# Performance work log

Measured on AMD Instinct MI355X. Metric: run time of the kernel, lower is better.

## Reference

```python
import jax, jax.numpy as jnp
import numpy as np

H, C = 2, 128  # heads, per-head channels
NEG_SLOPE = 0.2

N_FACT, N_STATUTE, N_CHARGE = 50000, 2000, 200
D_FACT, D_STATUTE, D_CHARGE = 768, 256, 128
E_M, E_I = 500000, 20000
NUM_CHARGES = 10


def setup_inputs() -> dict:
    key = jax.random.key(0)
    ks = iter(jax.random.split(key, 64))
    d = {}
    d['x_fact'] = jax.random.normal(next(ks), (N_FACT, D_FACT), jnp.float32)
    d['x_statute'] = jax.random.normal(next(ks), (N_STATUTE, D_STATUTE), jnp.float32)
    d['x_charge'] = jax.random.normal(next(ks), (N_CHARGE, D_CHARGE), jnp.float32)

    def gat_params(d_src, d_dst):
        s = 1.0 / np.sqrt(max(d_src, 1))
        return (jax.random.normal(next(ks), (d_src, H * C), jnp.float32) * s,
                jax.random.normal(next(ks), (d_dst, H * C), jnp.float32) * (1.0 / np.sqrt(d_dst)),
                jax.random.normal(next(ks), (H, C), jnp.float32) * 0.1,
                jax.random.normal(next(ks), (H, C), jnp.float32) * 0.1,
                jnp.zeros((H * C,), jnp.float32))
    # relation params: m = fact->statute, rm = statute->fact, i = statute->charge, ri = charge->statute
    (d['Wsrc_m'], d['Wdst_m'], d['asrc_m'], d['adst_m'], d['b_m']) = gat_params(D_FACT, D_STATUTE)
    (d['Wsrc_rm'], d['Wdst_rm'], d['asrc_rm'], d['adst_rm'], d['b_rm']) = gat_params(D_STATUTE, D_FACT)
    (d['Wsrc_i'], d['Wdst_i'], d['asrc_i'], d['adst_i'], d['b_i']) = gat_params(D_STATUTE, D_CHARGE)
    (d['Wsrc_ri'], d['Wdst_ri'], d['asrc_ri'], d['adst_ri'], d['b_ri']) = gat_params(D_CHARGE, D_STATUTE)
    d['Wc'] = jax.random.normal(next(ks), (H * C, NUM_CHARGES), jnp.float32) * (1.0 / np.sqrt(H * C))
    d['bc'] = jnp.zeros((NUM_CHARGES,), jnp.float32)

    d['m_src'] = jax.random.randint(next(ks), (E_M,), 0, N_FACT, jnp.int32)
    d['m_dst'] = jax.random.randint(next(ks), (E_M,), 0, N_STATUTE, jnp.int32)
    d['rm_src'] = jax.random.randint(next(ks), (E_M,), 0, N_STATUTE, jnp.int32)
    d['rm_dst'] = jax.random.randint(next(ks), (E_M,), 0, N_FACT, jnp.int32)
    d['i_src'] = jax.random.randint(next(ks), (E_I,), 0, N_STATUTE, jnp.int32)
    d['i_dst'] = jax.random.randint(next(ks), (E_I,), 0, N_CHARGE, jnp.int32)
    d['ri_src'] = jax.random.randint(next(ks), (E_I,), 0, N_CHARGE, jnp.int32)
    d['ri_dst'] = jax.random.randint(next(ks), (E_I,), 0, N_STATUTE, jnp.int32)
    return d


def gat_conv(xs, xd, Wsrc, Wdst, asrc, adst, bias, src, dst, n_dst):
    # bipartite GATConv, heads=2, concat=True, add_self_loops=False
    hs = (xs @ Wsrc).reshape(-1, H, C)          # [Ns,H,C]
    hd = (xd @ Wdst).reshape(-1, H, C)          # [Nd,H,C]
    als = jnp.einsum('nhc,hc->nh', hs, asrc)    # [Ns,H]
    ald = jnp.einsum('nhc,hc->nh', hd, adst)    # [Nd,H]
    e = jax.nn.leaky_relu(als[src] + ald[dst], NEG_SLOPE)  # [E,H]
    mx = jax.ops.segment_max(e, dst, num_segments=n_dst)
    ex = jnp.exp(e - mx[dst])
    denom = jax.ops.segment_sum(ex, dst, num_segments=n_dst)
    alpha = ex / (denom[dst] + 1e-16)           # segment softmax over dst groups
    msg = alpha[:, :, None] * hs[src]           # [E,H,C]
    out = jax.ops.segment_sum(msg, dst, num_segments=n_dst)
    return out.reshape(n_dst, H * C) + bias


def reference(x_fact, x_statute, x_charge,
              Wsrc_m, Wdst_m, asrc_m, adst_m, b_m,
              Wsrc_rm, Wdst_rm, asrc_rm, adst_rm, b_rm,
              Wsrc_i, Wdst_i, asrc_i, adst_i, b_i,
              Wsrc_ri, Wdst_ri, asrc_ri, adst_ri, b_ri,
              Wc, bc,
              m_src, m_dst, rm_src, rm_dst, i_src, i_dst, ri_src, ri_dst):
    out_st_m = gat_conv(x_fact, x_statute, Wsrc_m, Wdst_m, asrc_m, adst_m, b_m, m_src, m_dst, N_STATUTE)
    out_st_ri = gat_conv(x_charge, x_statute, Wsrc_ri, Wdst_ri, asrc_ri, adst_ri, b_ri, ri_src, ri_dst, N_STATUTE)
    statute_emb = 0.5 * (out_st_m + out_st_ri)  # HeteroConv aggr='mean' (unused downstream)
    fact_emb = gat_conv(x_statute, x_fact, Wsrc_rm, Wdst_rm, asrc_rm, adst_rm, b_rm, rm_src, rm_dst, N_FACT)
    charge_emb = gat_conv(x_statute, x_charge, Wsrc_i, Wdst_i, asrc_i, adst_i, b_i, i_src, i_dst, N_CHARGE)
    del statute_emb, charge_emb  # computed by the module but not used by classifier
    return fact_emb @ Wc + bc    # [N_FACT, NUM_CHARGES]
```

## Files before the change

kernel.cpp:

```cpp
#include <hip/hip_runtime.h>
#include <math.h>

#define NFACT 50000
#define NST   2000
#define DFACT 768
#define HC    256
#define EM    500000
#define NK    10
#define NEG   0.2f
#define NCHUNK 196

__device__ __forceinline__ float lrelu(float x) { return x > 0.f ? x : NEG * x; }

__global__ __launch_bounds__(256) void k_prep(const float* __restrict__ xs,
                                              const float* __restrict__ Wsrc,
                                              const float* __restrict__ asrc,
                                              const float* __restrict__ Wc,
                                              const float* __restrict__ Wdst,
                                              const float* __restrict__ adst,
                                              const float* __restrict__ b_rm,
                                              const float* __restrict__ bc,
                                              float* __restrict__ als,
                                              float* __restrict__ hsW,
                                              float* __restrict__ V,
                                              float* __restrict__ cst,
                                              int* __restrict__ counts) {
    int b = blockIdx.x, t = threadIdx.x;
    if (b < NST) {
        __shared__ float xrow[256];
        __shared__ float hrow[256];
        __shared__ float wsum[4];
        xrow[t] = xs[b * 256 + t];
        __syncthreads();
        float acc = 0.f;
        for (int d = 0; d < 256; ++d) acc += xrow[d] * Wsrc[d * 256 + t];
        float p = acc * asrc[t];
        for (int o = 32; o; o >>= 1) p += __shfl_xor(p, o, 64);
        hrow[t] = acc;
        if ((t & 63) == 0) wsum[t >> 6] = p;
        __syncthreads();
        if (t < 20) {
            int h = t / 10, k = t - h * 10;
            float a = 0.f;
            int base = h * 128;
            for (int c = 0; c < 128; ++c) a += hrow[base + c] * Wc[(base + c) * NK + k];
            hsW[b * 20 + t] = a;
        }
        if (t == 0) { als[b * 2 + 0] = wsum[0] + wsum[1]; als[b * 2 + 1] = wsum[2] + wsum[3]; }
    } else if (b < NST + 6) {
        int i = (b - NST) * 256 + t;
        if (i < DFACT * 2) {
            int d = i >> 1, h = i & 1;
            float acc = 0.f;
            for (int c = 0; c < 128; ++c)
                acc += Wdst[d * 256 + h * 128 + c] * adst[h * 128 + c];
            V[d * 2 + h] = acc;
        }
    } else if (b == NST + 6) {
        if (t < NK) {
            float a = bc[t];
            for (int ch = 0; ch < HC; ++ch) a += b_rm[ch] * Wc[ch * NK + t];
            cst[t] = a;
        }
    } else {
        int i = (b - (NST + 7)) * 256 + t;
        if (i <= NFACT) counts[i] = 0;
    }
}

__global__ void k_hist(const int* __restrict__ dst, int* __restrict__ counts) {
    int e = blockIdx.x * 256 + threadIdx.x;
    if (e < EM) atomicAdd(&counts[dst[e]], 1);
}

__global__ __launch_bounds__(256) void k_scanA(const int* __restrict__ counts,
                                               int* __restrict__ bsum) {
    __shared__ int sd[4];
    int t = threadIdx.x, i = blockIdx.x * 256 + t;
    int c = (i <= NFACT) ? counts[i] : 0;
    int v = c;
    for (int o = 32; o; o >>= 1) v += __shfl_xor(v, o, 64);
    if ((t & 63) == 0) sd[t >> 6] = v;
    __syncthreads();
    if (t == 0) bsum[blockIdx.x] = sd[0] + sd[1] + sd[2] + sd[3];
}

__global__ __launch_bounds__(256) void k_scanBC(const int* __restrict__ counts,
                                                const int* __restrict__ bsum,
                                                int* __restrict__ offs,
                                                int* __restrict__ cursor) {
    __shared__ int sb[256];
    __shared__ int sd[256];
    int t = threadIdx.x, b = blockIdx.x;
    sb[t] = (t < NCHUNK) ? bsum[t] : 0;
    __syncthreads();
    for (int o = 1; o < 256; o <<= 1) {
        int v = (t >= o) ? sb[t - o] : 0;
        __syncthreads();
        sb[t] += v;
        __syncthreads();
    }
    int myoff = (b > 0) ? sb[b - 1] : 0;
    int i = b * 256 + t;
    int c = (i <= NFACT) ? counts[i] : 0;
    sd[t] = c;
    __syncthreads();
    for (int o = 1; o < 256; o <<= 1) {
        int v = (t >= o) ? sd[t - o] : 0;
        __syncthreads();
        sd[t] += v;
        __syncthreads();
    }
    if (i <= NFACT) {
        int excl = myoff + sd[t] - c;
        offs[i] = excl;
        cursor[i] = excl;
    }
}

__global__ void k_scat(const int* __restrict__ src, const int* __restrict__ dst,
                       int* __restrict__ cursor, int* __restrict__ perm_s) {
    int e = blockIdx.x * 256 + threadIdx.x;
    if (e >= EM) return;
    int d = dst[e];
    int pos = atomicAdd(&cursor[d], 1);
    perm_s[pos] = src[e];
}

__global__ __launch_bounds__(256) void k_agg(const float* __restrict__ xf,
                                             const float* __restrict__ V,
                                             const float* __restrict__ hsW,
                                             const int* __restrict__ offs,
                                             const int* __restrict__ perm_s,
                                             const float2* __restrict__ als2,
                                             const float* __restrict__ cst,
                                             float* __restrict__ out) {
    int lane = threadIdx.x & 63, wid = threadIdx.x >> 6;
    int n = blockIdx.x * 4 + wid;

    const float* row = xf + (size_t)n * DFACT;
    float a0 = 0.f, a1 = 0.f;
    #pragma unroll
    for (int r = 0; r < 3; ++r) {
        int j0 = r * 256 + lane * 4;
        const float4 u = *(const float4*)(row + j0);
        a0 += u.x * V[(j0 + 0) * 2 + 0] + u.y * V[(j0 + 1) * 2 + 0]
            + u.z * V[(j0 + 2) * 2 + 0] + u.w * V[(j0 + 3) * 2 + 0];
        a1 += u.x * V[(j0 + 0) * 2 + 1] + u.y * V[(j0 + 1) * 2 + 1]
            + u.z * V[(j0 + 2) * 2 + 1] + u.w * V[(j0 + 3) * 2 + 1];
    }
    for (int o = 32; o; o >>= 1) { a0 += __shfl_xor(a0, o, 64); a1 += __shfl_xor(a1, o, 64); }

    bool live = lane < 20;
    bool h0   = lane < 10;
    float al = h0 ? a0 : a1;
    int beg = offs[n], end = offs[n + 1];

    float acc = 0.f, den = 0.f;
    int j = beg;
    for (; j + 4 <= end; j += 4) {
        int sA = perm_s[j + 0], sB = perm_s[j + 1], sC = perm_s[j + 2], sD = perm_s[j + 3];
        float2 aA = als2[sA], aB = als2[sB], aC = als2[sC], aD = als2[sD];
        float hA = live ? hsW[sA * 20 + lane] : 0.f;
        float hB = live ? hsW[sB * 20 + lane] : 0.f;
        float hC = live ? hsW[sC * 20 + lane] : 0.f;
        float hD = live ? hsW[sD * 20 + lane] : 0.f;
        float wA = __expf(lrelu((h0 ? aA.x : aA.y) + al));
        float wB = __expf(lrelu((h0 ? aB.x : aB.y) + al));
        float wC = __expf(lrelu((h0 ? aC.x : aC.y) + al));
        float wD = __expf(lrelu((h0 ? aD.x : aD.y) + al));
        den += (wA + wB) + (wC + wD);
        acc += wA * hA + wB * hB + wC * hC + wD * hD;
    }
    for (; j < end; ++j) {
        int s = perm_s[j];
        float2 a = als2[s];
        float h = live ? hsW[s * 20 + lane] : 0.f;
        float w = __expf(lrelu((h0 ? a.x : a.y) + al));
        den += w;
        acc += w * h;
    }
    float r = acc / (den + 1e-16f);
    float other = __shfl(r, (lane + 10) & 63, 64);
    if (h0) out[n * NK + lane] = r + other + cst[lane];
}

__global__ void k_sentinel(float* __restrict__ out, int n, float val) {
    int i = blockIdx.x * 256 + threadIdx.x;
    if (i < n) out[i] = val;
}

extern "C" void kernel_launch(void* const* d_in, const int* in_sizes, int n_in,
                              void* d_out, int out_size, void* d_ws, size_t ws_size,
                              hipStream_t stream) {
    const float* x_fact    = (const float*)d_in[0];
    const float* x_statute = (const float*)d_in[1];
    const float* Wsrc_rm   = (const float*)d_in[8];
    const float* Wdst_rm   = (const float*)d_in[9];
    const float* asrc_rm   = (const float*)d_in[10];
    const float* adst_rm   = (const float*)d_in[11];
    const float* b_rm      = (const float*)d_in[12];
    const float* Wc        = (const float*)d_in[23];
    const float* bc        = (const float*)d_in[24];
    const int* rm_src      = (const int*)d_in[27];
    const int* rm_dst      = (const int*)d_in[28];
    float* out = (float*)d_out;

    char* w0p = (char*)d_ws;
    char* w = w0p;
    auto carve = [&](size_t bytes) -> void* {
        void* p = (void*)w;
        w += (bytes + 511) & ~(size_t)511;
        return p;
    };
    float* als    = (float*)carve((size_t)NST * 2 * 4);
    float* hsW    = (float*)carve((size_t)NST * 20 * 4);
    float* V      = (float*)carve((size_t)DFACT * 2 * 4);
    float* cst    = (float*)carve(64);
    int*   counts = (int*)carve((size_t)(NFACT + 1) * 4);
    int*   offs   = (int*)carve((size_t)(NFACT + 1) * 4);
    int*   cursor = (int*)carve((size_t)(NFACT + 1) * 4);
    int*   bsum   = (int*)carve((size_t)NCHUNK * 4);
    int*   perm_s = (int*)carve((size_t)EM * 4);
    if ((size_t)(w - w0p) > ws_size) {
        k_sentinel<<<(out_size + 255) / 256, 256, 0, stream>>>(out, out_size, 2000.f);
        return;
    }

    k_prep<<<NST + 7 + NCHUNK, 256, 0, stream>>>(x_statute, Wsrc_rm, asrc_rm, Wc,
                                                 Wdst_rm, adst_rm, b_rm, bc,
                                                 als, hsW, V, cst, counts);
    k_hist<<<(EM + 255) / 256, 256, 0, stream>>>(rm_dst, counts);
    k_scanA<<<NCHUNK, 256, 0, stream>>>(counts, bsum);
    k_scanBC<<<NCHUNK, 256, 0, stream>>>(counts, bsum, offs, cursor);
    k_scat<<<(EM + 255) / 256, 256, 0, stream>>>(rm_src, rm_dst, cursor, perm_s);
    k_agg<<<NFACT / 4, 256, 0, stream>>>(x_fact, V, hsW, offs, perm_s,
                                         (const float2*)als, cst, out);
}
```

Before: 376.3 us.

## Fuse histogram into prep kernel and batch statute rows per block

```diff
diff --git a/kernel.cpp b/kernel.cpp
--- a/kernel.cpp
+++ b/kernel.cpp
@@ -9,46 +9,61 @@
 #define NK    10
 #define NEG   0.2f
 #define NCHUNK 196
+#define PB     1024
+#define HIST_B0 207
+
+typedef float vf4 __attribute__((ext_vector_type(4)));
 
 __device__ __forceinline__ float lrelu(float x) { return x > 0.f ? x : NEG * x; }
 
-__global__ __launch_bounds__(256) void k_prep(const float* __restrict__ xs,
-                                              const float* __restrict__ Wsrc,
-                                              const float* __restrict__ asrc,
-                                              const float* __restrict__ Wc,
-                                              const float* __restrict__ Wdst,
-                                              const float* __restrict__ adst,
-                                              const float* __restrict__ b_rm,
-                                              const float* __restrict__ bc,
-                                              float* __restrict__ als,
-                                              float* __restrict__ hsW,
-                                              float* __restrict__ V,
-                                              float* __restrict__ cst,
-                                              int* __restrict__ counts) {
+__global__ __launch_bounds__(256) void k_preph(const float* __restrict__ xs,
+                                               const float* __restrict__ Wsrc,
+                                               const float* __restrict__ asrc,
+                                               const float* __restrict__ Wc,
+                                               const float* __restrict__ Wdst,
+                                               const float* __restrict__ adst,
+                                               const float* __restrict__ b_rm,
+                                               const float* __restrict__ bc,
+                                               const int* __restrict__ dst,
+                                               float* __restrict__ als,
+                                               float* __restrict__ hsW,
+                                               float* __restrict__ V,
+                                               float* __restrict__ cst,
+                                               int* __restrict__ counts) {
     int b = blockIdx.x, t = threadIdx.x;
-    if (b < NST) {
+    if (b < 200) {
         __shared__ float xrow[256];
         __shared__ float hrow[256];
         __shared__ float wsum[4];
-        xrow[t] = xs[b * 256 + t];
-        __syncthreads();
-        float acc = 0.f;
-        for (int d = 0; d < 256; ++d) acc += xrow[d] * Wsrc[d * 256 + t];
-        float p = acc * asrc[t];
-        for (int o = 32; o; o >>= 1) p += __shfl_xor(p, o, 64);
-        hrow[t] = acc;
-        if ((t & 63) == 0) wsum[t >> 6] = p;
-        __syncthreads();
-        if (t < 20) {
-            int h = t / 10, k = t - h * 10;
-            float a = 0.f;
-            int base = h * 128;
-            for (int c = 0; c < 128; ++c) a += hrow[base + c] * Wc[(base + c) * NK + k];
-            hsW[b * 20 + t] = a;
+        for (int rr = 0; rr < 10; ++rr) {
+            int s = b * 10 + rr;
+            xrow[t] = xs[s * 256 + t];
+            __syncthreads();
+            float acc = 0.f;
+            for (int d = 0; d < 256; ++d) acc += xrow[d] * Wsrc[d * 256 + t];
+            float p = acc * asrc[t];
+            for (int o = 32; o; o >>= 1) p += __shfl_xor(p, o, 64);
+            hrow[t] = acc;
+            if ((t & 63) == 0) wsum[t >> 6] = p;
+            __syncthreads();
+            if (t < 20) {
+                int h = t / 10, k = t - h * 10;
+                float a = 0.f;
+                int base = h * 128;
+                for (int c = 0; c < 128; ++c) a += hrow[base + c] * Wc[(base + c) * NK + k];
+                hsW[s * 20 + t] = a;
+            }
+            if (t == 0) { als[s * 2 + 0] = wsum[0] + wsum[1]; als[s * 2 + 1] = wsum[2] + wsum[3]; }
+            __syncthreads();
         }
-        if (t == 0) { als[b * 2 + 0] = wsum[0] + wsum[1]; als[b * 2 + 1] = wsum[2] + wsum[3]; }
-    } else if (b < NST + 6) {
-        int i = (b - NST) * 256 + t;
+    } else if (b == 200) {
+        if (t < NK) {
+            float a = bc[t];
+            for (int ch = 0; ch < HC; ++ch) a += b_rm[ch] * Wc[ch * NK + t];
+            cst[t] = a;
+        }
+    } else if (b < HIST_B0) {
+        int i = (b - 201) * 256 + t;
         if (i < DFACT * 2) {
             int d = i >> 1, h = i & 1;
             float acc = 0.f;
@@ -56,21 +71,11 @@
                 acc += Wdst[d * 256 + h * 128 + c] * adst[h * 128 + c];
             V[d * 2 + h] = acc;
         }
-    } else if (b == NST + 6) {
-        if (t < NK) {
-            float a = bc[t];
-            for (int ch = 0; ch < HC; ++ch) a += b_rm[ch] * Wc[ch * NK + t];
-            cst[t] = a;
-        }
     } else {
-        int i = (b - (NST + 7)) * 256 + t;
-        if (i <= NFACT) counts[i] = 0;
-    }
-}
-
-__global__ void k_hist(const int* __restrict__ dst, int* __restrict__ counts) {
-    int e = blockIdx.x * 256 + threadIdx.x;
-    if (e < EM) atomicAdd(&counts[dst[e]], 1);
+        const int stride = (PB - HIST_B0) * 256;
+        for (int e = (b - HIST_B0) * 256 + t; e < EM; e += stride)
+            atomicAdd(&counts[dst[e]], 1);
+    }
 }
 
 __global__ __launch_bounds__(256) void k_scanA(const int* __restrict__ counts,
@@ -135,7 +140,8 @@
                                              const float2* __restrict__ als2,
                                              const float* __restrict__ cst,
                                              float* __restrict__ out) {
-    int lane = threadIdx.x & 63, wid = threadIdx.x >> 6;
+    int lane = threadIdx.x & 63;
+    int wid = __builtin_amdgcn_readfirstlane(threadIdx.x >> 6);
     int n = blockIdx.x * 4 + wid;
 
     const float* row = xf + (size_t)n * DFACT;
@@ -143,7 +149,7 @@
     #pragma unroll
     for (int r = 0; r < 3; ++r) {
         int j0 = r * 256 + lane * 4;
-        const float4 u = *(const float4*)(row + j0);
+        const vf4 u = __builtin_nontemporal_load((const vf4*)(row + j0));
         a0 += u.x * V[(j0 + 0) * 2 + 0] + u.y * V[(j0 + 1) * 2 + 0]
             + u.z * V[(j0 + 2) * 2 + 0] + u.w * V[(j0 + 3) * 2 + 0];
         a1 += u.x * V[(j0 + 0) * 2 + 1] + u.y * V[(j0 + 1) * 2 + 1]
@@ -227,10 +233,11 @@
         return;
     }
 
-    k_prep<<<NST + 7 + NCHUNK, 256, 0, stream>>>(x_statute, Wsrc_rm, asrc_rm, Wc,
-                                                 Wdst_rm, adst_rm, b_rm, bc,
-                                                 als, hsW, V, cst, counts);
-    k_hist<<<(EM + 255) / 256, 256, 0, stream>>>(rm_dst, counts);
+    (void)hipMemsetAsync(counts, 0, (size_t)(NFACT + 1) * 4, stream);
+
+    k_preph<<<PB, 256, 0, stream>>>(x_statute, Wsrc_rm, asrc_rm, Wc,
+                                    Wdst_rm, adst_rm, b_rm, bc, rm_dst,
+                                    als, hsW, V, cst, counts);
     k_scanA<<<NCHUNK, 256, 0, stream>>>(counts, bsum);
     k_scanBC<<<NCHUNK, 256, 0, stream>>>(counts, bsum, offs, cursor);
     k_scat<<<(EM + 255) / 256, 256, 0, stream>>>(rm_src, rm_dst, cursor, perm_s);
```

New measurement: 403.6 us. 7.3% more time.
